# Performance work log

Hardware: AMD Instinct MI355X
Metric: run time of the kernel (lower is better)

## Reference

```python
import jax, jax.numpy as jnp
import numpy as np

B, C1, C2, H, W = 8, 256, 256, 64, 64
C = 256            # int(c1*e)
G = C // 16        # 16 groups (dg)
Cg = C // G        # 16 channels per group
K = 9              # 3x3 kernel sample points
BN_EPS = 1e-5

# kernel grid offsets for 3x3, dilation 1 (pad=1 centers the grid)
KH = jnp.array([-1, -1, -1, 0, 0, 0, 1, 1, 1], jnp.float32)
KW = jnp.array([-1, 0, 1, -1, 0, 1, -1, 0, 1], jnp.float32)


def setup_inputs() -> dict:
    key = jax.random.key(0)
    ks = jax.random.split(key, 10)
    x = jax.random.normal(ks[0], (B, C1, H, W), jnp.float32)
    w_cv1 = jax.random.normal(ks[1], (C, C1), jnp.float32) / np.sqrt(C1)
    b_cv1 = jax.random.normal(ks[2], (C,), jnp.float32) * 0.1
    # offset/mask linear (DCNv4 inits to zero; small scale keeps sampling sane)
    w_off = jax.random.normal(ks[3], (G * 3 * K, C), jnp.float32) * 0.01
    b_off = jax.random.normal(ks[4], (G * 3 * K,), jnp.float32) * 0.01
    w_cv2 = jax.random.normal(ks[5], (C2, C), jnp.float32) / np.sqrt(C)
    bn_gamma = jax.random.uniform(ks[6], (C2,), jnp.float32, 0.5, 1.5)
    bn_beta = jax.random.normal(ks[7], (C2,), jnp.float32) * 0.1
    bn_mean = jax.random.normal(ks[8], (C2,), jnp.float32) * 0.1
    bn_var = jax.random.uniform(ks[9], (C2,), jnp.float32, 0.5, 1.5)
    return dict(x=x, w_cv1=w_cv1, b_cv1=b_cv1, w_off=w_off, b_off=b_off,
                w_cv2=w_cv2, bn_gamma=bn_gamma, bn_beta=bn_beta,
                bn_mean=bn_mean, bn_var=bn_var)


def _gather(vflat, hi, wi):
    # vflat: (B, H*W, G, Cg); hi/wi: (B,H,W,K,G) float corner indices
    ok = ((hi >= 0) & (hi < H) & (wi >= 0) & (wi < W)).astype(vflat.dtype)
    idx = (jnp.clip(hi, 0, H - 1) * W + jnp.clip(wi, 0, W - 1)).astype(jnp.int32)
    idx = idx.reshape(B, H * W * K, G)
    idxb = jnp.broadcast_to(idx[..., None], (B, H * W * K, G, Cg))
    g = jnp.take_along_axis(vflat, idxb, axis=1)  # (B, HWK, G, Cg)
    return g.reshape(B, H, W, K, G, Cg), ok


def _dcnv4(v, off, mask):
    # v: (B,H,W,G,Cg); off: (B,H,W,G,K,2) (dh,dw); mask: (B,H,W,G,K)
    ii = jnp.arange(H, dtype=jnp.float32)
    jj = jnp.arange(W, dtype=jnp.float32)
    ph = ii[None, :, None, None, None] + KH[None, None, None, None, :] + off[..., 0]
    pw = jj[None, None, :, None, None] + KW[None, None, None, None, :] + off[..., 1]
    ph = ph.transpose(0, 1, 2, 4, 3)  # (B,H,W,K,G)
    pw = pw.transpose(0, 1, 2, 4, 3)
    h0 = jnp.floor(ph); w0 = jnp.floor(pw)
    ah = ph - h0; aw = pw - w0
    vflat = v.reshape(B, H * W, G, Cg)
    g00, ok00 = _gather(vflat, h0, w0)
    g01, ok01 = _gather(vflat, h0, w0 + 1)
    g10, ok10 = _gather(vflat, h0 + 1, w0)
    g11, ok11 = _gather(vflat, h0 + 1, w0 + 1)
    w00 = ((1 - ah) * (1 - aw) * ok00)[..., None]
    w01 = ((1 - ah) * aw * ok01)[..., None]
    w10 = (ah * (1 - aw) * ok10)[..., None]
    w11 = (ah * aw * ok11)[..., None]
    sample = w00 * g00 + w01 * g01 + w10 * g10 + w11 * g11  # (B,H,W,K,G,Cg)
    out = jnp.einsum('bhwkgc,bhwgk->bhwgc', sample, mask)
    return out.reshape(B, H, W, C).transpose(0, 3, 1, 2)  # NCHW


def reference(x, w_cv1, b_cv1, w_off, b_off, w_cv2, bn_gamma, bn_beta, bn_mean, bn_var):
    # cv1: 1x1 conv
    h1 = jnp.einsum('bchw,oc->bohw', x, w_cv1) + b_cv1[None, :, None, None]
    # offset/mask 1x1 projection, per-group layout [2K offsets, K masks]
    om = jnp.einsum('bchw,oc->bhwo', h1, w_off) + b_off
    om = om.reshape(B, H, W, G, 3 * K)
    off = om[..., :2 * K].reshape(B, H, W, G, K, 2)
    mask = om[..., 2 * K:]  # DCNv4: no softmax, used directly
    v = h1.transpose(0, 2, 3, 1).reshape(B, H, W, G, Cg)
    y = _dcnv4(v, off, mask)
    # cv2: 1x1 conv (no bias)
    y = jnp.einsum('bchw,oc->bohw', y, w_cv2)
    # BatchNorm (eval mode)
    scale = (bn_gamma / jnp.sqrt(bn_var + BN_EPS))[None, :, None, None]
    y = (y - bn_mean[None, :, None, None]) * scale + bn_beta[None, :, None, None]
    # SiLU
    return y * jax.nn.sigmoid(y)
```

## Files before the change

kernel.cpp:

```cpp
#include <hip/hip_runtime.h>

#define HW 4096
#define CCH 256
#define MOFF 432
#define PTOT 32768
#define PDIM 68
#define PIMG (PDIM*PDIM)

typedef unsigned short u16;
typedef __attribute__((ext_vector_type(8))) short short8;
typedef __attribute__((ext_vector_type(8))) unsigned short u16x8;
typedef __attribute__((ext_vector_type(4))) unsigned short u16x4;
typedef __attribute__((ext_vector_type(4))) float f32x4;

__device__ __forceinline__ u16 f2b(float f){
  unsigned int u = __float_as_uint(f);
  unsigned int rounding = 0x7FFFu + ((u >> 16) & 1u);
  return (u16)((u + rounding) >> 16);
}
__device__ __forceinline__ float b2f(u16 s){
  return __uint_as_float(((unsigned int)s) << 16);
}

__global__ __launch_bounds__(256) void k_cvtw(const float* __restrict__ w1,
    const float* __restrict__ woff, const float* __restrict__ w2,
    const float* __restrict__ gamma, const float* __restrict__ beta,
    const float* __restrict__ mean, const float* __restrict__ var,
    u16* __restrict__ wb1, u16* __restrict__ wboff, u16* __restrict__ wb2,
    float* __restrict__ bnA, float* __restrict__ bnB, u16* __restrict__ h1p){
  int r = blockIdx.x, t = threadIdx.x;
  if (r < 256) wb1[r*256 + t] = f2b(w1[r*256 + t]);
  else if (r < 704){ int o = r - 256; wboff[o*256 + t] = (o < MOFF) ? f2b(woff[o*256 + t]) : (u16)0; }
  else if (r < 960){ int o = r - 704; wb2[o*256 + t] = f2b(w2[o*256 + t]); }
  else if (r == 960){
    if (t < 256){
      float sc = gamma[t] * rsqrtf(var[t] + 1e-5f);
      bnA[t] = sc;
      bnB[t] = beta[t] - mean[t] * sc;
    }
  } else {
    int n = (r - 961) * 128 + (t >> 1);
    int seg = t & 1;
    int plane = n / 528, m = n % 528;
    int row, col;
    if (m < 136){ row = m / 68; col = m % 68; }
    else if (m < 272){ int mm = m - 136; row = 66 + mm / 68; col = mm % 68; }
    else { int mm = m - 272; row = 2 + (mm >> 2); int c4 = mm & 3; col = (c4 & 1) + 66 * (c4 >> 1); }
    u16x8 z = {};
    *reinterpret_cast<u16x8*>(&h1p[((size_t)plane * PIMG + row * PDIM + col) * 16 + seg * 8]) = z;
  }
}

__global__ __launch_bounds__(256) void k_xt(const float* __restrict__ x,
    u16* __restrict__ xT){
  __shared__ float tile[64][65];
  const int pb = blockIdx.x * 64, cb = blockIdx.y * 64, b = blockIdx.z;
  const int t = threadIdx.x;
  const float* src = x + ((size_t)(b * CCH + cb)) * HW + pb;
  #pragma unroll
  for (int pass = 0; pass < 4; ++pass){
    int c_l = pass * 16 + (t >> 4);
    int pq = (t & 15) * 4;
    float4 v = *reinterpret_cast<const float4*>(&src[(size_t)c_l * HW + pq]);
    tile[pq + 0][c_l] = v.x; tile[pq + 1][c_l] = v.y;
    tile[pq + 2][c_l] = v.z; tile[pq + 3][c_l] = v.w;
  }
  __syncthreads();
  #pragma unroll
  for (int pass = 0; pass < 4; ++pass){
    int p_l = pass * 16 + (t >> 4);
    int cq = (t & 15) * 4;
    u16x4 o4;
    #pragma unroll
    for (int j = 0; j < 4; ++j) o4[j] = f2b(tile[p_l][cq + j]);
    *reinterpret_cast<u16x4*>(&xT[((size_t)b * HW + pb + p_l) * CCH + cb + cq]) = o4;
  }
}

template<int BN, bool GUARD, bool SILU, int AMODE, bool PADC>
__global__ __launch_bounds__(256) void k_gemm(const void* __restrict__ Asrc,
    const u16* __restrict__ Bw, const float* __restrict__ bias,
    const float* __restrict__ bnB, void* __restrict__ Cout, int ldc, int NL){
  constexpr int WN = BN / 2;
  constexpr int MF = 4;
  constexpr int NF = WN / 16;
  constexpr int BOFF = 128 * 40;
  constexpr int STG = (128 + BN) * 40;
  constexpr int CMAT = 128 * (BN + 8);
  constexpr int SM = SILU ? STG : (STG > CMAT ? STG : CMAT);
  __shared__ __align__(16) u16 smem[SM];

  const int t = threadIdx.x;
  const int tm = blockIdx.x * 128;
  const int tn = blockIdx.y * BN;
  const int lane = t & 63;
  const int wid = t >> 6;
  const int wr = wid >> 1, wc = wid & 1;

  f32x4 acc[MF][NF] = {};

  for (int kc = 0; kc < 256; kc += 32){
    if constexpr (AMODE == 2){
      const u16* Ap = (const u16*)Asrc;
      #pragma unroll
      for (int i = 0; i < 2; ++i){
        int v = t + i * 256;
        int row = v >> 2, cq = v & 3;
        int p = tm + row;
        int bb = p >> 12, ii = (p >> 6) & 63, jj = p & 63;
        int c = kc + cq * 8;
        size_t base = ((size_t)(bb * 16 + (c >> 4)) * PIMG + (ii + 2) * PDIM + jj + 2) * 16 + (c & 15);
        *reinterpret_cast<u16x8*>(&smem[row * 40 + cq * 8]) =
          *reinterpret_cast<const u16x8*>(&Ap[base]);
      }
    } else {
      const u16* Ap = (const u16*)Asrc;
      #pragma unroll
      for (int i = 0; i < 2; ++i){
        int v = t + i * 256;
        int row = v >> 2, cq = v & 3;
        *reinterpret_cast<u16x8*>(&smem[row * 40 + cq * 8]) =
          *reinterpret_cast<const u16x8*>(&Ap[(size_t)(tm + row) * 256 + kc + cq * 8]);
      }
    }
    constexpr int BV = BN * 4 / 256;
    #pragma unroll
    for (int i = 0; i < BV; ++i){
      int v = t + i * 256;
      int row = v >> 2, cq = v & 3;
      *reinterpret_cast<u16x8*>(&smem[BOFF + row * 40 + cq * 8]) =
        *reinterpret_cast<const u16x8*>(&Bw[(size_t)(tn + row) * 256 + kc + cq * 8]);
    }
    __syncthreads();
    short8 af[MF], bf[NF];
    #pragma unroll
    for (int m = 0; m < MF; ++m)
      af[m] = *reinterpret_cast<const short8*>(
        &smem[(wr * 64 + m * 16 + (lane & 15)) * 40 + (lane >> 4) * 8]);
    #pragma unroll
    for (int n = 0; n < NF; ++n)
      bf[n] = *reinterpret_cast<const short8*>(
        &smem[BOFF + (wc * WN + n * 16 + (lane & 15)) * 40 + (lane >> 4) * 8]);
    #pragma unroll
    for (int m = 0; m < MF; ++m)
      #pragma unroll
      for (int n = 0; n < NF; ++n)
        acc[m][n] = __builtin_amdgcn_mfma_f32_16x16x32_bf16(af[m], bf[n], acc[m][n], 0, 0, 0);
    __syncthreads();
  }

  if constexpr (SILU){
    const int bimg = tm >> 12;
    const int ploc = tm & 4095;
    float* outp = (float*)Cout;
    #pragma unroll
    for (int n = 0; n < NF; ++n){
      int o = tn + wc * WN + n * 16 + (lane & 15);
      float sA = bias[o], sB = bnB[o];
      #pragma unroll
      for (int m = 0; m < MF; ++m){
        int prow = wr * 64 + m * 16 + ((lane >> 4) << 2);
        f32x4 st;
        #pragma unroll
        for (int j = 0; j < 4; ++j){
          float y = acc[m][n][j] * sA + sB;
          st[j] = y / (1.f + expf(-y));
        }
        *reinterpret_cast<f32x4*>(&outp[((size_t)(bimg * 256 + o)) * HW + ploc + prow]) = st;
      }
    }
  } else {
    constexpr int CP = BN + 8;
    u16* C_l = smem;
    #pragma unroll
    for (int n = 0; n < NF; ++n){
      int col = wc * WN + n * 16 + (lane & 15);
      int o = tn + col;
      float bi = (!GUARD || o < NL) ? bias[o] : 0.f;
      #pragma unroll
      for (int m = 0; m < MF; ++m){
        int r0 = wr * 64 + m * 16 + ((lane >> 4) << 2);
        #pragma unroll
        for (int j = 0; j < 4; ++j)
          C_l[(r0 + j) * CP + col] = f2b(acc[m][n][j] + bi);
      }
    }
    __syncthreads();
    constexpr int SEG = BN / 8;
    constexpr int RPP = 256 / SEG;
    u16* Co = (u16*)Cout;
    #pragma unroll
    for (int pass = 0; pass < 128 / RPP; ++pass){
      int row = pass * RPP + t / SEG;
      int sg = t % SEG;
      int oc = tn + sg * 8;
      if constexpr (PADC){
        int p = tm + row;
        int bb = p >> 12, ii = (p >> 6) & 63, jj = p & 63;
        size_t dst = ((size_t)(bb * 16 + (oc >> 4)) * PIMG + (ii + 2) * PDIM + jj + 2) * 16 + (oc & 15);
        *reinterpret_cast<u16x8*>(&Co[dst]) =
          *reinterpret_cast<const u16x8*>(&C_l[row * CP + sg * 8]);
      } else {
        if (!GUARD || oc + 8 <= NL)
          *reinterpret_cast<u16x8*>(&Co[(size_t)(tm + row) * ldc + oc]) =
            *reinterpret_cast<const u16x8*>(&C_l[row * CP + sg * 8]);
      }
    }
  }
}

__global__ __launch_bounds__(256) void k_sample(const u16* __restrict__ h1p,
    const u16* __restrict__ om, u16* __restrict__ ydcn){
  __shared__ float oms[4 * MOFF];
  const int t = threadIdx.x;
  const int pblk = blockIdx.x * 4;
  if (t < 216){
    u16x8 v = *reinterpret_cast<const u16x8*>(&om[(size_t)pblk * MOFF + t * 8]);
    float4 lo, hi;
    lo.x = b2f(v[0]); lo.y = b2f(v[1]); lo.z = b2f(v[2]); lo.w = b2f(v[3]);
    hi.x = b2f(v[4]); hi.y = b2f(v[5]); hi.z = b2f(v[6]); hi.w = b2f(v[7]);
    *reinterpret_cast<float4*>(&oms[t * 8]) = lo;
    *reinterpret_cast<float4*>(&oms[t * 8 + 4]) = hi;
  }
  __syncthreads();

  const int px = t >> 6;
  const int g = (t >> 2) & 15;
  const int q = t & 3;
  const int p = pblk + px;
  const int b = p >> 12, hw = p & 4095;
  const int ic = hw >> 6, jc = hw & 63;
  const u16* plane = h1p + (size_t)(b * 16 + g) * PIMG * 16;
  const float* ob = &oms[px * MOFF + g * 27];
  const float fi = (float)ic, fj = (float)jc;
  const bool wsel = (q >= 2);

  float acc[8] = {};
  #pragma unroll
  for (int k = 0; k < 9; ++k){
    float oh = ob[2 * k], ow = ob[2 * k + 1], m = ob[18 + k];
    float ph = fi + (float)(k / 3 - 1) + oh;
    float pw = fj + (float)(k % 3 - 1) + ow;
    float h0f = floorf(ph), w0f = floorf(pw);
    float ah = ph - h0f, aw = pw - w0f;
    int h0 = (int)h0f, w0 = (int)w0f;
    int hc = min(max(h0, -2), 64) + 2;
    int wc = min(max(w0, -2), 64) + 2;
    const u16* cbase = plane + ((hc * PDIM + wc) << 4) + (q << 3);
    u16x8 tv = *reinterpret_cast<const u16x8*>(cbase);
    u16x8 bv = *reinterpret_cast<const u16x8*>(cbase + PDIM * 16);
    float mh1 = m * ah, mh0 = m - mh1;
    float awq = wsel ? aw : (1.f - aw);
    float ct = mh0 * awq, cb = mh1 * awq;
    #pragma unroll
    for (int j = 0; j < 8; ++j)
      acc[j] += ct * b2f(tv[j]) + cb * b2f(bv[j]);
  }
  #pragma unroll
  for (int j = 0; j < 8; ++j)
    acc[j] += __shfl_xor(acc[j], 2, 64);
  if (q < 2){
    u16x8 o8;
    #pragma unroll
    for (int j = 0; j < 8; ++j) o8[j] = f2b(acc[j]);
    *reinterpret_cast<u16x8*>(&ydcn[(size_t)p * 256 + g * 16 + q * 8]) = o8;
  }
}

extern "C" void kernel_launch(void* const* d_in, const int* in_sizes, int n_in,
                              void* d_out, int out_size, void* d_ws, size_t ws_size,
                              hipStream_t stream) {
  const float* x     = (const float*)d_in[0];
  const float* w1    = (const float*)d_in[1];
  const float* b1    = (const float*)d_in[2];
  const float* woff  = (const float*)d_in[3];
  const float* boff  = (const float*)d_in[4];
  const float* w2    = (const float*)d_in[5];
  const float* gamma = (const float*)d_in[6];
  const float* beta  = (const float*)d_in[7];
  const float* mean  = (const float*)d_in[8];
  const float* var   = (const float*)d_in[9];
  float* out = (float*)d_out;
  (void)in_sizes; (void)n_in; (void)out_size; (void)ws_size;

  u16* h1p   = (u16*)d_ws;
  u16* om    = h1p + (size_t)128 * PIMG * 16;
  u16* xT    = om + (size_t)PTOT * MOFF;
  u16* ydcn  = xT;
  u16* wb1   = xT + (size_t)PTOT * CCH;
  u16* wboff = wb1 + 256 * 256;
  u16* wb2   = wboff + 448 * 256;
  float* bnA = (float*)(wb2 + 256 * 256);
  float* bnB = bnA + 256;

  dim3 blk(256);
  k_cvtw<<<dim3(1489), blk, 0, stream>>>(w1, woff, w2, gamma, beta, mean, var,
                                         wb1, wboff, wb2, bnA, bnB, h1p);
  k_xt<<<dim3(64, 4, 8), blk, 0, stream>>>(x, xT);
  k_gemm<128, false, false, 0, true><<<dim3(PTOT / 128, 2), blk, 0, stream>>>(
      (const void*)xT, wb1, b1, nullptr, (void*)h1p, 0, 256);
  k_gemm<64, true, false, 2, false><<<dim3(PTOT / 128, 7), blk, 0, stream>>>(
      (const void*)h1p, wboff, boff, nullptr, (void*)om, MOFF, MOFF);
  k_sample<<<dim3(PTOT / 4), blk, 0, stream>>>(h1p, om, ydcn);
  k_gemm<128, false, true, 0, false><<<dim3(PTOT / 128, 2), blk, 0, stream>>>(
      (const void*)ydcn, wb2, bnA, bnB, (void*)out, 0, 256);
}
```

Measured before the change: 105.0 us.

## Fold offset projection into cv1 weights and run both GEMMs as one launch

Precomputes combined weights W_off·W1 and bias W_off·b1+b_off in a new small kernel. cv1 and the offset/mask projection then become a single GEMM over xT with 768 output columns, writing h1 to the padded layout and om to its own buffer. This removes the second GEMM's read of h1p and one kernel launch, at the cost of extra MFMA work from the K=256 input side. Block indices are remapped so tiles are spread across XCDs. Numerics change slightly because the combined weights are rounded to bf16 and om no longer goes through the bf16-rounded h1.

Result: no change. 104.4 us (-0.5%).

```diff
diff --git a/kernel.cpp b/kernel.cpp
--- a/kernel.cpp
+++ b/kernel.cpp
@@ -23,23 +23,23 @@
 }
 
 __global__ __launch_bounds__(256) void k_cvtw(const float* __restrict__ w1,
-    const float* __restrict__ woff, const float* __restrict__ w2,
+    const float* __restrict__ w2,
     const float* __restrict__ gamma, const float* __restrict__ beta,
     const float* __restrict__ mean, const float* __restrict__ var,
-    u16* __restrict__ wb1, u16* __restrict__ wboff, u16* __restrict__ wb2,
+    u16* __restrict__ wb_big, u16* __restrict__ wb2,
     float* __restrict__ bnA, float* __restrict__ bnB, u16* __restrict__ h1p){
   int r = blockIdx.x, t = threadIdx.x;
-  if (r < 256) wb1[r*256 + t] = f2b(w1[r*256 + t]);
-  else if (r < 704){ int o = r - 256; wboff[o*256 + t] = (o < MOFF) ? f2b(woff[o*256 + t]) : (u16)0; }
-  else if (r < 960){ int o = r - 704; wb2[o*256 + t] = f2b(w2[o*256 + t]); }
-  else if (r == 960){
+  if (r < 256) wb_big[r*256 + t] = f2b(w1[r*256 + t]);
+  else if (r < 336){ wb_big[(688 + (r - 256)) * 256 / 1 + t] = 0; }
+  else if (r < 592){ int o = r - 336; wb2[o*256 + t] = f2b(w2[o*256 + t]); }
+  else if (r == 592){
     if (t < 256){
       float sc = gamma[t] * rsqrtf(var[t] + 1e-5f);
       bnA[t] = sc;
       bnB[t] = beta[t] - mean[t] * sc;
     }
   } else {
-    int n = (r - 961) * 128 + (t >> 1);
+    int n = (r - 593) * 128 + (t >> 1);
     int seg = t & 1;
     int plane = n / 528, m = n % 528;
     int row, col;
@@ -51,6 +51,28 @@
   }
 }
 
+__global__ __launch_bounds__(256) void k_wcomb(const float* __restrict__ w1,
+    const float* __restrict__ woff, const float* __restrict__ b1,
+    const float* __restrict__ boff,
+    u16* __restrict__ wb_big, float* __restrict__ bcomb){
+  __shared__ float wr_[256];
+  __shared__ float pb[256];
+  const int j = blockIdx.x, t = threadIdx.x;
+  wr_[t] = woff[j * 256 + t];
+  __syncthreads();
+  float s = 0.f;
+  #pragma unroll 8
+  for (int m = 0; m < 256; ++m) s += wr_[m] * w1[m * 256 + t];
+  wb_big[(256 + j) * 256 + t] = f2b(s);
+  pb[t] = wr_[t] * b1[t];
+  __syncthreads();
+  if (t == 0){
+    float bs = boff[j];
+    for (int m = 0; m < 256; ++m) bs += pb[m];
+    bcomb[j] = bs;
+  }
+}
+
 __global__ __launch_bounds__(256) void k_xt(const float* __restrict__ x,
     u16* __restrict__ xT){
   __shared__ float tile[64][65];
@@ -77,134 +99,157 @@
   }
 }
 
-template<int BN, bool GUARD, bool SILU, int AMODE, bool PADC>
-__global__ __launch_bounds__(256) void k_gemm(const void* __restrict__ Asrc,
-    const u16* __restrict__ Bw, const float* __restrict__ bias,
-    const float* __restrict__ bnB, void* __restrict__ Cout, int ldc, int NL){
-  constexpr int WN = BN / 2;
-  constexpr int MF = 4;
-  constexpr int NF = WN / 16;
-  constexpr int BOFF = 128 * 40;
-  constexpr int STG = (128 + BN) * 40;
-  constexpr int CMAT = 128 * (BN + 8);
-  constexpr int SM = SILU ? STG : (STG > CMAT ? STG : CMAT);
-  __shared__ __align__(16) u16 smem[SM];
+__global__ __launch_bounds__(256) void k_gemm_big(const u16* __restrict__ A,
+    const u16* __restrict__ Bw, const float* __restrict__ b1,
+    const float* __restrict__ bcomb, u16* __restrict__ h1p,
+    u16* __restrict__ om){
+  __shared__ __align__(16) u16 smem[128 * 136];
+  const int bid = blockIdx.x;
+  const int xcd = bid & 7, s = bid >> 3;
+  const int row_local = s / 6, cblk = s % 6;
+  const int tm = (row_local * 8 + xcd) * 128;
+  const int tn = cblk * 128;
 
   const int t = threadIdx.x;
-  const int tm = blockIdx.x * 128;
-  const int tn = blockIdx.y * BN;
   const int lane = t & 63;
   const int wid = t >> 6;
   const int wr = wid >> 1, wc = wid & 1;
-
-  f32x4 acc[MF][NF] = {};
+  constexpr int BOFF = 128 * 40;
+
+  f32x4 acc[4][4] = {};
 
   for (int kc = 0; kc < 256; kc += 32){
-    if constexpr (AMODE == 2){
-      const u16* Ap = (const u16*)Asrc;
-      #pragma unroll
-      for (int i = 0; i < 2; ++i){
-        int v = t + i * 256;
-        int row = v >> 2, cq = v & 3;
-        int p = tm + row;
-        int bb = p >> 12, ii = (p >> 6) & 63, jj = p & 63;
-        int c = kc + cq * 8;
-        size_t base = ((size_t)(bb * 16 + (c >> 4)) * PIMG + (ii + 2) * PDIM + jj + 2) * 16 + (c & 15);
-        *reinterpret_cast<u16x8*>(&smem[row * 40 + cq * 8]) =
-          *reinterpret_cast<const u16x8*>(&Ap[base]);
-      }
-    } else {
-      const u16* Ap = (const u16*)Asrc;
-      #pragma unroll
-      for (int i = 0; i < 2; ++i){
-        int v = t + i * 256;
-        int row = v >> 2, cq = v & 3;
-        *reinterpret_cast<u16x8*>(&smem[row * 40 + cq * 8]) =
-          *reinterpret_cast<const u16x8*>(&Ap[(size_t)(tm + row) * 256 + kc + cq * 8]);
-      }
-    }
-    constexpr int BV = BN * 4 / 256;
-    #pragma unroll
-    for (int i = 0; i < BV; ++i){
+    #pragma unroll
+    for (int i = 0; i < 2; ++i){
+      int v = t + i * 256;
+      int row = v >> 2, cq = v & 3;
+      *reinterpret_cast<u16x8*>(&smem[row * 40 + cq * 8]) =
+        *reinterpret_cast<const u16x8*>(&A[(size_t)(tm + row) * 256 + kc + cq * 8]);
+    }
+    #pragma unroll
+    for (int i = 0; i < 2; ++i){
       int v = t + i * 256;
       int row = v >> 2, cq = v & 3;
       *reinterpret_cast<u16x8*>(&smem[BOFF + row * 40 + cq * 8]) =
         *reinterpret_cast<const u16x8*>(&Bw[(size_t)(tn + row) * 256 + kc + cq * 8]);
     }
     __syncthreads();
-    short8 af[MF], bf[NF];
-    #pragma unroll
-    for (int m = 0; m < MF; ++m)
+    short8 af[4], bf[4];
+    #pragma unroll
+    for (int m = 0; m < 4; ++m)
       af[m] = *reinterpret_cast<const short8*>(
         &smem[(wr * 64 + m * 16 + (lane & 15)) * 40 + (lane >> 4) * 8]);
     #pragma unroll
-    for (int n = 0; n < NF; ++n)
+    for (int n = 0; n < 4; ++n)
       bf[n] = *reinterpret_cast<const short8*>(
-        &smem[BOFF + (wc * WN + n * 16 + (lane & 15)) * 40 + (lane >> 4) * 8]);
-    #pragma unroll
-    for (int m = 0; m < MF; ++m)
+        &smem[BOFF + (wc * 64 + n * 16 + (lane & 15)) * 40 + (lane >> 4) * 8]);
+    #pragma unroll
+    for (int m = 0; m < 4; ++m)
       #pragma unroll
-      for (int n = 0; n < NF; ++n)
+      for (int n = 0; n < 4; ++n)
         acc[m][n] = __builtin_amdgcn_mfma_f32_16x16x32_bf16(af[m], bf[n], acc[m][n], 0, 0, 0);
     __syncthreads();
   }
 
-  if constexpr (SILU){
-    const int bimg = tm >> 12;
-    const int ploc = tm & 4095;
-    float* outp = (float*)Cout;
-    #pragma unroll
-    for (int n = 0; n < NF; ++n){
-      int o = tn + wc * WN + n * 16 + (lane & 15);
-      float sA = bias[o], sB = bnB[o];
+  constexpr int CP = 136;
+  u16* C_l = smem;
+  #pragma unroll
+  for (int n = 0; n < 4; ++n){
+    int col = wc * 64 + n * 16 + (lane & 15);
+    int o = tn + col;
+    float bi = (o < 256) ? b1[o] : ((o - 256 < MOFF) ? bcomb[o - 256] : 0.f);
+    #pragma unroll
+    for (int m = 0; m < 4; ++m){
+      int r0 = wr * 64 + m * 16 + ((lane >> 4) << 2);
       #pragma unroll
-      for (int m = 0; m < MF; ++m){
-        int prow = wr * 64 + m * 16 + ((lane >> 4) << 2);
-        f32x4 st;
-        #pragma unroll
-        for (int j = 0; j < 4; ++j){
-          float y = acc[m][n][j] * sA + sB;
-          st[j] = y / (1.f + expf(-y));
-        }
-        *reinterpret_cast<f32x4*>(&outp[((size_t)(bimg * 256 + o)) * HW + ploc + prow]) = st;
+      for (int j = 0; j < 4; ++j)
+        C_l[(r0 + j) * CP + col] = f2b(acc[m][n][j] + bi);
+    }
+  }
+  __syncthreads();
+  #pragma unroll
+  for (int pass = 0; pass < 8; ++pass){
+    int row = pass * 16 + (t >> 4);
+    int sg = t & 15;
+    int oc = tn + sg * 8;
+    int p = tm + row;
+    if (tn < 256){
+      int bb = p >> 12, ii = (p >> 6) & 63, jj = p & 63;
+      size_t dst = ((size_t)(bb * 16 + (oc >> 4)) * PIMG + (ii + 2) * PDIM + jj + 2) * 16 + (oc & 15);
+      *reinterpret_cast<u16x8*>(&h1p[dst]) =
+        *reinterpret_cast<const u16x8*>(&C_l[row * CP + sg * 8]);
+    } else {
+      int occ = oc - 256;
+      if (occ + 8 <= MOFF)
+        *reinterpret_cast<u16x8*>(&om[(size_t)p * MOFF + occ]) =
+          *reinterpret_cast<const u16x8*>(&C_l[row * CP + sg * 8]);
+    }
+  }
+}
+
+__global__ __launch_bounds__(256) void k_gemm2(const u16* __restrict__ A,
+    const u16* __restrict__ Bw, const float* __restrict__ bnA,
+    const float* __restrict__ bnB, float* __restrict__ out){
+  __shared__ __align__(16) u16 smem[(128 + 128) * 40];
+  const int t = threadIdx.x;
+  const int tm = blockIdx.x * 128;
+  const int tn = blockIdx.y * 128;
+  const int lane = t & 63;
+  const int wid = t >> 6;
+  const int wr = wid >> 1, wc = wid & 1;
+  constexpr int BOFF = 128 * 40;
+
+  f32x4 acc[4][4] = {};
+
+  for (int kc = 0; kc < 256; kc += 32){
+    #pragma unroll
+    for (int i = 0; i < 2; ++i){
+      int v = t + i * 256;
+      int row = v >> 2, cq = v & 3;
+      *reinterpret_cast<u16x8*>(&smem[row * 40 + cq * 8]) =
+        *reinterpret_cast<const u16x8*>(&A[(size_t)(tm + row) * 256 + kc + cq * 8]);
+    }
+    #pragma unroll
+    for (int i = 0; i < 2; ++i){
+      int v = t + i * 256;
+      int row = v >> 2, cq = v & 3;
+      *reinterpret_cast<u16x8*>(&smem[BOFF + row * 40 + cq * 8]) =
+        *reinterpret_cast<const u16x8*>(&Bw[(size_t)(tn + row) * 256 + kc + cq * 8]);
+    }
+    __syncthreads();
+    short8 af[4], bf[4];
+    #pragma unroll
+    for (int m = 0; m < 4; ++m)
+      af[m] = *reinterpret_cast<const short8*>(
+        &smem[(wr * 64 + m * 16 + (lane & 15)) * 40 + (lane >> 4) * 8]);
+    #pragma unroll
+    for (int n = 0; n < 4; ++n)
+      bf[n] = *reinterpret_cast<const short8*>(
+        &smem[BOFF + (wc * 64 + n * 16 + (lane & 15)) * 40 + (lane >> 4) * 8]);
+    #pragma unroll
+    for (int m = 0; m < 4; ++m)
+      #pragma unroll
+      for (int n = 0; n < 4; ++n)
+        acc[m][n] = __builtin_amdgcn_mfma_f32_16x16x32_bf16(af[m], bf[n], acc[m][n], 0, 0, 0);
+    __syncthreads();
+  }
+
+  const int bimg = tm >> 12;
+  const int ploc = tm & 4095;
+  #pragma unroll
+  for (int n = 0; n < 4; ++n){
+    int o = tn + wc * 64 + n * 16 + (lane & 15);
+    float sA = bnA[o], sB = bnB[o];
+    #pragma unroll
+    for (int m = 0; m < 4; ++m){
+      int prow = wr * 64 + m * 16 + ((lane >> 4) << 2);
+      f32x4 st;
+      #pragma unroll
+      for (int j = 0; j < 4; ++j){
+        float y = acc[m][n][j] * sA + sB;
+        st[j] = y / (1.f + expf(-y));
       }
-    }
-  } else {
-    constexpr int CP = BN + 8;
-    u16* C_l = smem;
-    #pragma unroll
-    for (int n = 0; n < NF; ++n){
-      int col = wc * WN + n * 16 + (lane & 15);
-      int o = tn + col;
-      float bi = (!GUARD || o < NL) ? bias[o] : 0.f;
-      #pragma unroll
-      for (int m = 0; m < MF; ++m){
-        int r0 = wr * 64 + m * 16 + ((lane >> 4) << 2);
-        #pragma unroll
-        for (int j = 0; j < 4; ++j)
-          C_l[(r0 + j) * CP + col] = f2b(acc[m][n][j] + bi);
-      }
-    }
-    __syncthreads();
-    constexpr int SEG = BN / 8;
-    constexpr int RPP = 256 / SEG;
-    u16* Co = (u16*)Cout;
-    #pragma unroll
-    for (int pass = 0; pass < 128 / RPP; ++pass){
-      int row = pass * RPP + t / SEG;
-      int sg = t % SEG;
-      int oc = tn + sg * 8;
-      if constexpr (PADC){
-        int p = tm + row;
-        int bb = p >> 12, ii = (p >> 6) & 63, jj = p & 63;
-        size_t dst = ((size_t)(bb * 16 + (oc >> 4)) * PIMG + (ii + 2) * PDIM + jj + 2) * 16 + (oc & 15);
-        *reinterpret_cast<u16x8*>(&Co[dst]) =
-          *reinterpret_cast<const u16x8*>(&C_l[row * CP + sg * 8]);
-      } else {
-        if (!GUARD || oc + 8 <= NL)
-          *reinterpret_cast<u16x8*>(&Co[(size_t)(tm + row) * ldc + oc]) =
-            *reinterpret_cast<const u16x8*>(&C_l[row * CP + sg * 8]);
-      }
+      *reinterpret_cast<f32x4*>(&out[((size_t)(bimg * 256 + o)) * HW + ploc + prow]) = st;
     }
   }
 }
@@ -283,25 +328,22 @@
   float* out = (float*)d_out;
   (void)in_sizes; (void)n_in; (void)out_size; (void)ws_size;
 
-  u16* h1p   = (u16*)d_ws;
-  u16* om    = h1p + (size_t)128 * PIMG * 16;
-  u16* xT    = om + (size_t)PTOT * MOFF;
-  u16* ydcn  = xT;
-  u16* wb1   = xT + (size_t)PTOT * CCH;
-  u16* wboff = wb1 + 256 * 256;
-  u16* wb2   = wboff + 448 * 256;
-  float* bnA = (float*)(wb2 + 256 * 256);
-  float* bnB = bnA + 256;
+  u16* h1p    = (u16*)d_ws;
+  u16* om     = h1p + (size_t)128 * PIMG * 16;
+  u16* xT     = om + (size_t)PTOT * MOFF;
+  u16* ydcn   = xT;
+  u16* wb_big = xT + (size_t)PTOT * CCH;
+  u16* wb2    = wb_big + 768 * 256;
+  float* bnA  = (float*)(wb2 + 256 * 256);
+  float* bnB  = bnA + 256;
+  float* bcomb = bnB + 256;
 
   dim3 blk(256);
-  k_cvtw<<<dim3(1489), blk, 0, stream>>>(w1, woff, w2, gamma, beta, mean, var,
-                                         wb1, wboff, wb2, bnA, bnB, h1p);
+  k_cvtw<<<dim3(1121), blk, 0, stream>>>(w1, w2, gamma, beta, mean, var,
+                                         wb_big, wb2, bnA, bnB, h1p);
+  k_wcomb<<<dim3(432), blk, 0, stream>>>(w1, woff, b1, boff, wb_big, bcomb);
   k_xt<<<dim3(64, 4, 8), blk, 0, stream>>>(x, xT);
-  k_gemm<128, false, false, 0, true><<<dim3(PTOT / 128, 2), blk, 0, stream>>>(
-      (const void*)xT, wb1, b1, nullptr, (void*)h1p, 0, 256);
-  k_gemm<64, true, false, 2, false><<<dim3(PTOT / 128, 7), blk, 0, stream>>>(
-      (const void*)h1p, wboff, boff, nullptr, (void*)om, MOFF, MOFF);
+  k_gemm_big<<<dim3(1536), blk, 0, stream>>>(xT, wb_big, b1, bcomb, h1p, om);
   k_sample<<<dim3(PTOT / 4), blk, 0, stream>>>(h1p, om, ydcn);
-  k_gemm<128, false, true, 0, false><<<dim3(PTOT / 128, 2), blk, 0, stream>>>(
-      (const void*)ydcn, wb2, bnA, bnB, (void*)out, 0, 256);
-}
+  k_gemm2<<<dim3(PTOT / 128, 2), blk, 0, stream>>>(ydcn, wb2, bnA, bnB, out);
+}
```
